# Kernel optimization log

Measured on AMD Instinct MI355X. Metric: run time of the kernel, lower is better.

The kernel has to match this reference:

```python
import jax, jax.numpy as jnp
import numpy as np

B, C, H, W = 16, 128, 64, 64
LN_EPS = 1e-5


def _gru_dir(x, w_ih, w_hh, b_ih, b_hh, reverse):
    # x: [N, T, C]; PyTorch GRU cell math:
    # r = sig(Wir x + bir + Whr h + bhr); z = sig(Wiz x + biz + Whz h + bhz)
    xp = jnp.einsum('ntc,gc->ntg', x, w_ih) + b_ih  # [N,T,3C] precomputed input gates
    xs = jnp.swapaxes(xp, 0, 1)  # [T,N,3C]
    h0 = jnp.zeros((x.shape[0], w_hh.shape[1]), x.dtype)

    def step(h, xt):
        g = h @ w_hh.T + b_hh
        xr, xz, xn = jnp.split(xt, 3, axis=-1)
        hr, hz, hn = jnp.split(g, 3, axis=-1)
        r = jax.nn.sigmoid(xr + hr)
        z = jax.nn.sigmoid(xz + hz)
        n = jnp.tanh(xn + r * hn)
        h2 = (1.0 - z) * n + z * h
        return h2, h2

    _, ys = jax.lax.scan(step, h0, xs, reverse=reverse)
    return jnp.swapaxes(ys, 0, 1)  # [N,T,C]


def _gru_bidir(x, wih_f, whh_f, bih_f, bhh_f, wih_b, whh_b, bib_b, bhh_b):
    of = _gru_dir(x, wih_f, whh_f, bih_f, bhh_f, False)
    ob = _gru_dir(x, wih_b, whh_b, bib_b, bhh_b, True)
    return jnp.concatenate([of, ob], axis=-1)  # [N,T,2C]


def _forward(x, ln_g, ln_b,
             h_wih_f, h_whh_f, h_bih_f, h_bhh_f,
             h_wih_b, h_whh_b, h_bih_b, h_bhh_b,
             w_wih_f, w_whh_f, w_bih_f, w_bhh_f,
             w_wih_b, w_whh_b, w_bih_b, w_bhh_b,
             proj_w, proj_b):
    Bn, Cc, Hh, Ww = x.shape
    x_flat = x.reshape(Bn, Cc, Hh * Ww).transpose(0, 2, 1)  # b (h w) c
    mu = x_flat.mean(-1, keepdims=True)
    var = ((x_flat - mu) ** 2).mean(-1, keepdims=True)
    xn = (x_flat - mu) * jax.lax.rsqrt(var + LN_EPS) * ln_g + ln_b
    x4 = xn.reshape(Bn, Hh, Ww, Cc)
    # horizontal scan: rows as batch, sequence along W
    x_h = x4.reshape(Bn * Hh, Ww, Cc)
    out_h = _gru_bidir(x_h, h_wih_f, h_whh_f, h_bih_f, h_bhh_f,
                       h_wih_b, h_whh_b, h_bih_b, h_bhh_b)
    out_h = out_h.reshape(Bn, Hh * Ww, 2 * Cc)
    # vertical scan: cols as batch, sequence along H
    x_v = x4.transpose(0, 2, 1, 3).reshape(Bn * Ww, Hh, Cc)
    out_v = _gru_bidir(x_v, w_wih_f, w_whh_f, w_bih_f, w_bhh_f,
                       w_wih_b, w_whh_b, w_bih_b, w_bhh_b)
    out_v = out_v.reshape(Bn, Ww, Hh, 2 * Cc).transpose(0, 2, 1, 3).reshape(Bn, Hh * Ww, 2 * Cc)
    out = jnp.concatenate([out_h, out_v], axis=-1) @ proj_w.T + proj_b
    out = out + x_flat  # dropout in eval mode = identity
    return out.transpose(0, 2, 1).reshape(Bn, Cc, Hh, Ww)


def setup_inputs():
    key = jax.random.key(0)
    key, kx = jax.random.split(key)
    d = {
        'x': jax.random.normal(kx, (B, C, H, W), jnp.float32),
        'ln_g': jnp.ones((C,), jnp.float32),
        'ln_b': jnp.zeros((C,), jnp.float32),
    }
    bound = 1.0 / np.sqrt(C)  # torch GRU init: U(-1/sqrt(hidden), 1/sqrt(hidden))
    shapes = {'wih': (3 * C, C), 'whh': (3 * C, C), 'bih': (3 * C,), 'bhh': (3 * C,)}
    for pre in ('h', 'w'):
        for dr in ('f', 'b'):
            for p, sh in shapes.items():
                key, k1 = jax.random.split(key)
                d[f'{pre}_{p}_{dr}'] = jax.random.uniform(k1, sh, jnp.float32, -bound, bound)
    bp = 1.0 / np.sqrt(4 * C)
    key, k1, k2 = jax.random.split(key, 3)
    d['proj_w'] = jax.random.uniform(k1, (C, 4 * C), jnp.float32, -bp, bp)
    d['proj_b'] = jax.random.uniform(k2, (C,), jnp.float32, -bp, bp)
    return d


def reference(x, ln_g, ln_b,
              h_wih_f, h_whh_f, h_bih_f, h_bhh_f,
              h_wih_b, h_whh_b, h_bih_b, h_bhh_b,
              w_wih_f, w_whh_f, w_bih_f, w_bhh_f,
              w_wih_b, w_whh_b, w_bih_b, w_bhh_b,
              proj_w, proj_b):
    return _forward(x, ln_g, ln_b,
                    h_wih_f, h_whh_f, h_bih_f, h_bhh_f,
                    h_wih_b, h_whh_b, h_bih_b, h_bhh_b,
                    w_wih_f, w_whh_f, w_bih_f, w_bhh_f,
                    w_wih_b, w_whh_b, w_bih_b, w_bhh_b,
                    proj_w, proj_b)
```

## Files before the change

kernel.cpp:

```cpp
#include <hip/hip_runtime.h>

typedef short bf16x8 __attribute__((ext_vector_type(8)));
typedef float f32x4 __attribute__((ext_vector_type(4)));

static __device__ __forceinline__ unsigned short f2bf(float f) {
  unsigned u = __builtin_bit_cast(unsigned, f);
  u += 0x7FFFu + ((u >> 16) & 1u);
  return (unsigned short)(u >> 16);
}

static __device__ __forceinline__ bf16x8 pack8s(const float* p, float s) {
  float4 a = *(const float4*)p;
  float4 b = *(const float4*)(p + 4);
  bf16x8 r;
  r[0] = (short)f2bf(a.x * s); r[1] = (short)f2bf(a.y * s);
  r[2] = (short)f2bf(a.z * s); r[3] = (short)f2bf(a.w * s);
  r[4] = (short)f2bf(b.x * s); r[5] = (short)f2bf(b.y * s);
  r[6] = (short)f2bf(b.z * s); r[7] = (short)f2bf(b.w * s);
  return r;
}

#define NLOG2E -1.442695040888963f
#define N2LOG2E -2.885390081777927f

__global__ __launch_bounds__(512) void pwprep_kernel(
    const float* __restrict__ pw, unsigned short* __restrict__ pwb) {
  const int i = blockIdx.x * 512 + threadIdx.x;
  pwb[i] = f2bf(pw[i]);
}

__global__ __launch_bounds__(512, 2) void ln_kernel(
    const float* __restrict__ x, const float* __restrict__ lg,
    const float* __restrict__ lb, unsigned short* __restrict__ xn) {
  __shared__ __align__(16) unsigned char slds[35840];
  float* mu_s = (float*)(slds + 34816);
  float* rs_s = (float*)(slds + 35328);
  const int tid = threadIdx.x;
  const int bid = blockIdx.x;
  const int b = bid >> 5;
  const int hw0 = (bid & 31) << 7;
  const int q = tid >> 5, slot = tid & 31;
  const int lane = tid & 63, wv = tid >> 6;

  const float* xbase = x + ((size_t)b * 128) * 4096 + hw0 + (slot << 2);
  float4 xv[8];
#pragma unroll
  for (int p = 0; p < 8; ++p)
    xv[p] = *(const float4*)(xbase + (size_t)(q * 8 + p) * 4096);

  float s1[4] = {0.f, 0.f, 0.f, 0.f}, s2[4] = {0.f, 0.f, 0.f, 0.f};
#pragma unroll
  for (int p = 0; p < 8; ++p) {
    s1[0] += xv[p].x; s2[0] = fmaf(xv[p].x, xv[p].x, s2[0]);
    s1[1] += xv[p].y; s2[1] = fmaf(xv[p].y, xv[p].y, s2[1]);
    s1[2] += xv[p].z; s2[2] = fmaf(xv[p].z, xv[p].z, s2[2]);
    s1[3] += xv[p].w; s2[3] = fmaf(xv[p].w, xv[p].w, s2[3]);
  }
#pragma unroll
  for (int j = 0; j < 4; ++j) {
    s1[j] += __shfl_xor(s1[j], 32);
    s2[j] += __shfl_xor(s2[j], 32);
  }
  if (lane < 32) {
    float* psp = (float*)(slds + (wv * 32 + slot) * 36);
#pragma unroll
    for (int j = 0; j < 4; ++j) { psp[j] = s1[j]; psp[4 + j] = s2[j]; }
  }
  __syncthreads();
  if (tid < 128) {
    const int sl2 = tid >> 2, j2 = tid & 3;
    float a1 = 0.f, a2 = 0.f;
#pragma unroll
    for (int w = 0; w < 8; ++w) {
      const float* psp = (const float*)(slds + (w * 32 + sl2) * 36);
      a1 += psp[j2]; a2 += psp[4 + j2];
    }
    const float mu = a1 * 0.0078125f;
    const float var = a2 * 0.0078125f - mu * mu;
    mu_s[tid] = mu;
    rs_s[tid] = rsqrtf(var + 1e-5f);
  }
  __syncthreads();

  float lgv[8], lbv[8];
#pragma unroll
  for (int p = 0; p < 8; ++p) { lgv[p] = lg[q * 8 + p]; lbv[p] = lb[q * 8 + p]; }
#pragma unroll
  for (int j = 0; j < 4; ++j) {
    const int pos = (slot << 2) + j;
    const float mu = mu_s[pos], rs = rs_s[pos];
    float y[8];
#pragma unroll
    for (int p = 0; p < 8; ++p) {
      const float xvj = j == 0 ? xv[p].x : j == 1 ? xv[p].y : j == 2 ? xv[p].z : xv[p].w;
      y[p] = (xvj - mu) * rs * lgv[p] + lbv[p];
    }
    unsigned h0, h1, h2, h3;
    asm("v_cvt_pk_bf16_f32 %0, %1, %2" : "=v"(h0) : "v"(y[0]), "v"(y[1]));
    asm("v_cvt_pk_bf16_f32 %0, %1, %2" : "=v"(h1) : "v"(y[2]), "v"(y[3]));
    asm("v_cvt_pk_bf16_f32 %0, %1, %2" : "=v"(h2) : "v"(y[4]), "v"(y[5]));
    asm("v_cvt_pk_bf16_f32 %0, %1, %2" : "=v"(h3) : "v"(y[6]), "v"(y[7]));
    uint4 v; v.x = h0; v.y = h1; v.z = h2; v.w = h3;
    *(uint4*)(slds + pos * 272 + (q << 4)) = v;
  }
  __syncthreads();
#pragma unroll
  for (int it = 0; it < 4; ++it) {
    const int idx = (it << 9) + tid;
    const int row = idx >> 4, g = idx & 15;
    uint4 v = *(const uint4*)(slds + row * 272 + (g << 4));
    *(uint4*)((unsigned char*)xn + ((size_t)(b * 4096 + hw0 + row)) * 256 + (g << 4)) = v;
  }
}

__global__ __launch_bounds__(512, 2) void scan_kernel(
    const unsigned short* __restrict__ xn, unsigned short* __restrict__ cat,
    const float* __restrict__ wih0, const float* __restrict__ whh0,
    const float* __restrict__ bih0, const float* __restrict__ bhh0,
    const float* __restrict__ wih1, const float* __restrict__ whh1,
    const float* __restrict__ bih1, const float* __restrict__ bhh1,
    const float* __restrict__ wih2, const float* __restrict__ whh2,
    const float* __restrict__ bih2, const float* __restrict__ bhh2,
    const float* __restrict__ wih3, const float* __restrict__ whh3,
    const float* __restrict__ bih3, const float* __restrict__ bhh3) {
  __shared__ __align__(16) unsigned char lds[16384];
  const int tid = threadIdx.x;
  const int bid = blockIdx.x;
  const int dir = bid >> 6;
  const int grp = bid & 63;
  const int fwd = !(dir & 1);
  const int vert = dir >> 1;
  const int b = grp >> 2;
  const int r0 = (grp & 3) << 4;
  const int wv = tid >> 6;
  const int lane = tid & 63;
  const int l15 = lane & 15;
  const int l4 = lane >> 4;

  const float* wih = dir == 0 ? wih0 : dir == 1 ? wih1 : dir == 2 ? wih2 : wih3;
  const float* whh = dir == 0 ? whh0 : dir == 1 ? whh1 : dir == 2 ? whh2 : whh3;
  const float* bih = dir == 0 ? bih0 : dir == 1 ? bih1 : dir == 2 ? bih2 : bih3;
  const float* bhh = dir == 0 ? bhh0 : dir == 1 ? bhh1 : dir == 2 ? bhh2 : bhh3;

  const int ca = (wv << 4) + l15;
  bf16x8 wf[3][2][4];
#pragma unroll
  for (int g = 0; g < 3; ++g) {
    const float sc = g == 2 ? N2LOG2E : NLOG2E;
#pragma unroll
    for (int s = 0; s < 2; ++s) {
      const float* Wp = s ? whh : wih;
#pragma unroll
      for (int kc = 0; kc < 4; ++kc)
        wf[g][s][kc] = pack8s(Wp + (size_t)((g << 7) + ca) * 128 + (kc << 5) + (l4 << 3), sc);
    }
  }
  const int cb = (wv << 4) + (l4 << 2);
  f32x4 br4, bz4, bnx4, bnh4;
  {
    float4 a = *(const float4*)(bih + cb), b2 = *(const float4*)(bhh + cb);
    br4[0] = (a.x + b2.x) * NLOG2E; br4[1] = (a.y + b2.y) * NLOG2E;
    br4[2] = (a.z + b2.z) * NLOG2E; br4[3] = (a.w + b2.w) * NLOG2E;
    a = *(const float4*)(bih + 128 + cb); b2 = *(const float4*)(bhh + 128 + cb);
    bz4[0] = (a.x + b2.x) * NLOG2E; bz4[1] = (a.y + b2.y) * NLOG2E;
    bz4[2] = (a.z + b2.z) * NLOG2E; bz4[3] = (a.w + b2.w) * NLOG2E;
    a = *(const float4*)(bih + 256 + cb);
    bnx4[0] = a.x * N2LOG2E; bnx4[1] = a.y * N2LOG2E;
    bnx4[2] = a.z * N2LOG2E; bnx4[3] = a.w * N2LOG2E;
    b2 = *(const float4*)(bhh + 256 + cb);
    bnh4[0] = b2.x * N2LOG2E; bnh4[1] = b2.y * N2LOG2E;
    bnh4[2] = b2.z * N2LOG2E; bnh4[3] = b2.w * N2LOG2E;
  }

  const int ss = tid >> 4, ck = tid & 15;
  const unsigned char* xsp =
      (const unsigned char*)xn +
      (vert ? ((size_t)b << 20) + (size_t)(r0 + ss) * 256 + (ck << 4)
            : ((size_t)(b * 64 + r0 + ss) << 14) + (ck << 4));
  const int xstep = vert ? 16384 : 256;
  const int sdst = (ss * 256 + (ck << 4)) ^ ((ss & 15) << 4);

  const int seq = r0 + l15;
  const int cstep = vert ? 65536 : 1024;
  unsigned char* catp =
      (unsigned char*)cat +
      ((size_t)b * 4096 + (size_t)(vert ? seq : seq * 64)) * 1024 + dir * 256 + (cb << 1) +
      (size_t)(fwd ? 0 : 63) * cstep;
  const int cdelta = fwd ? cstep : -cstep;

  *(unsigned long long*)(lds + 8192 + tid * 8) = 0ull;
  f32x4 hst = {0.f, 0.f, 0.f, 0.f};

  uint4 sX, sY;
  f32x4 grA, gzA, gnxA, grB, gzB, gnxB;
  {
    const unsigned char* xlq =
        (const unsigned char*)xn +
        (vert ? ((size_t)b << 20) + (size_t)(fwd ? 0 : 63) * 16384 + (size_t)seq * 256
              : ((size_t)(b * 64 + seq) << 14) + (size_t)(fwd ? 0 : 63) * 256) +
        (l4 << 4);
    bf16x8 x0[4];
#pragma unroll
    for (int kc = 0; kc < 4; ++kc) x0[kc] = *(const bf16x8*)(xlq + (kc << 6));
    uint4 s1v;
    if (tid < 256) {
      s1v = *(const uint4*)(xsp + (fwd ? 1 : 62) * xstep);
      sX = *(const uint4*)(xsp + (fwd ? 2 : 61) * xstep);
    }
    grA = br4; gzA = bz4; gnxA = bnx4;
#pragma unroll
    for (int kc = 0; kc < 4; ++kc) {
      grA = __builtin_amdgcn_mfma_f32_16x16x32_bf16(wf[0][0][kc], x0[kc], grA, 0, 0, 0);
      gzA = __builtin_amdgcn_mfma_f32_16x16x32_bf16(wf[1][0][kc], x0[kc], gzA, 0, 0, 0);
      gnxA = __builtin_amdgcn_mfma_f32_16x16x32_bf16(wf[2][0][kc], x0[kc], gnxA, 0, 0, 0);
    }
    if (tid < 256) *(uint4*)(lds + 4096 + sdst) = s1v;
  }
  __syncthreads();

#define STEP(TT, HCUR, HNXT, XRD, XWR, XW, XL, GRC, GZC, GNXC, GRN, GZN, GNXN)  \
  {                                                                             \
    bf16x8 ha[4], xa[4];                                                        \
    _Pragma("unroll")                                                           \
    for (int kc = 0; kc < 4; ++kc) {                                            \
      const int base = (l15 * 256 + (kc << 6) + (l4 << 4)) ^ (l15 << 4);        \
      ha[kc] = *(const bf16x8*)(lds + (HCUR) + base);                           \
      xa[kc] = *(const bf16x8*)(lds + (XRD) + base);                            \
    }                                                                           \
    if (tid < 256) {                                                            \
      *(uint4*)(lds + (XWR) + sdst) = XW;                                       \
      const int tl = (TT) + 3 > 63 ? 63 : (TT) + 3;                             \
      XL = *(const uint4*)(xsp + (fwd ? tl : 63 - tl) * xstep);                 \
    }                                                                           \
    f32x4 rh = {0.f, 0.f, 0.f, 0.f}, zh = {0.f, 0.f, 0.f, 0.f}, nh = bnh4;     \
    _Pragma("unroll")                                                           \
    for (int kc = 0; kc < 4; ++kc) {                                            \
      rh = __builtin_amdgcn_mfma_f32_16x16x32_bf16(wf[0][1][kc], ha[kc], rh, 0, 0, 0); \
      zh = __builtin_amdgcn_mfma_f32_16x16x32_bf16(wf[1][1][kc], ha[kc], zh, 0, 0, 0); \
      nh = __builtin_amdgcn_mfma_f32_16x16x32_bf16(wf[2][1][kc], ha[kc], nh, 0, 0, 0); \
    }                                                                           \
    GRN = br4; GZN = bz4; GNXN = bnx4;                                          \
    _Pragma("unroll")                                                           \
    for (int kc = 0; kc < 4; ++kc) {                                            \
      GRN = __builtin_amdgcn_mfma_f32_16x16x32_bf16(wf[0][0][kc], xa[kc], GRN, 0, 0, 0); \
      GZN = __builtin_amdgcn_mfma_f32_16x16x32_bf16(wf[1][0][kc], xa[kc], GZN, 0, 0, 0); \
      GNXN = __builtin_amdgcn_mfma_f32_16x16x32_bf16(wf[2][0][kc], xa[kc], GNXN, 0, 0, 0); \
    }                                                                           \
    f32x4 hnew;                                                                 \
    _Pragma("unroll")                                                           \
    for (int r = 0; r < 4; ++r) {                                               \
      const float er = __builtin_amdgcn_exp2f(GRC[r] + rh[r]);                  \
      const float rr = __builtin_amdgcn_rcpf(1.f + er);                         \
      const float ez = __builtin_amdgcn_exp2f(GZC[r] + zh[r]);                  \
      const float zz = __builtin_amdgcn_rcpf(1.f + ez);                         \
      const float pre = GNXC[r] + rr * nh[r];                                   \
      const float e2 = __builtin_amdgcn_exp2f(pre);                             \
      const float nn = fmaf(2.f, __builtin_amdgcn_rcpf(1.f + e2), -1.f);        \
      hnew[r] = nn + zz * (hst[r] - nn);                                        \
    }                                                                           \
    hst = hnew;                                                                 \
    unsigned hp0, hp1;                                                          \
    asm("v_cvt_pk_bf16_f32 %0, %1, %2" : "=v"(hp0) : "v"(hnew[0]), "v"(hnew[1])); \
    asm("v_cvt_pk_bf16_f32 %0, %1, %2" : "=v"(hp1) : "v"(hnew[2]), "v"(hnew[3])); \
    {                                                                           \
      unsigned long long hp = (unsigned long long)hp0 | ((unsigned long long)hp1 << 32); \
      *(unsigned long long*)(lds + (HNXT) + ((l15 * 256 + (cb << 1)) ^ (l15 << 4))) = hp; \
    }                                                                           \
    {                                                                           \
      uint2 v; v.x = hp0; v.y = hp1;                                            \
      *(uint2*)catp = v;                                                        \
      catp += cdelta;                                                           \
    }                                                                           \
    asm volatile("s_waitcnt lgkmcnt(0)" ::: "memory");                          \
    __builtin_amdgcn_s_barrier();                                               \
    asm volatile("" ::: "memory");                                              \
  }

  for (int tt2 = 0; tt2 < 64; tt2 += 2) {
    STEP(tt2, 8192, 12288, 4096, 0, sX, sY, grA, gzA, gnxA, grB, gzB, gnxB);
    STEP(tt2 + 1, 12288, 8192, 0, 4096, sY, sX, grB, gzB, gnxB, grA, gzA, gnxA);
  }
#undef STEP
}

__global__ __launch_bounds__(512, 4) void proj_kernel(
    const unsigned short* __restrict__ cat, const unsigned short* __restrict__ pwb,
    const float* __restrict__ pb, const float* __restrict__ x,
    float* __restrict__ out) {
  __shared__ __align__(16) unsigned char lds[33280];
  const int tid = threadIdx.x;
  const int bid = blockIdx.x;
  const int row0 = bid << 6;
  const int b = row0 >> 12;
  const int hw0 = row0 & 4095;
  const int wv = tid >> 6, lane = tid & 63, l15 = lane & 15, l4 = lane >> 4;

  const int cc = (wv << 4) + l15;
  bf16x8 wfr[16];
#pragma unroll
  for (int kc = 0; kc < 16; ++kc)
    wfr[kc] = *(const bf16x8*)(pwb + (size_t)cc * 512 + (kc << 5) + (l4 << 3));
  const float pbv = pb[cc];

  f32x4 acc[4];
#pragma unroll
  for (int mt = 0; mt < 4; ++mt) acc[mt] = {pbv, pbv, pbv, pbv};

#pragma unroll
  for (int s = 0; s < 2; ++s) {
#pragma unroll
    for (int it = 0; it < 4; ++it) {
      const int item = tid + (it << 9);
      const int rr = item >> 6, ckk = item & 63;
      uint4 v = *(const uint4*)((const unsigned char*)cat +
                                ((size_t)(row0 + (s << 5) + rr)) * 1024 + ckk * 16);
      *(uint4*)(lds + rr * 1024 + ((ckk ^ (rr & 7)) << 4)) = v;
    }
    __syncthreads();
#pragma unroll
    for (int mh = 0; mh < 2; ++mh) {
      const int mt = (s << 1) + mh;
      const int rl = (mh << 4) + l15;
#pragma unroll
      for (int kc = 0; kc < 16; ++kc) {
        bf16x8 af =
            *(const bf16x8*)(lds + rl * 1024 + ((((kc << 2) + l4) ^ (rl & 7)) << 4));
        acc[mt] = __builtin_amdgcn_mfma_f32_16x16x32_bf16(af, wfr[kc], acc[mt], 0, 0, 0);
      }
    }
    __syncthreads();
  }

#pragma unroll
  for (int mt = 0; mt < 4; ++mt)
#pragma unroll
    for (int j = 0; j < 4; ++j)
      *(float*)(lds + cc * 260 + (((mt << 4) + (l4 << 2) + j) << 2)) = acc[mt][j];
  __syncthreads();
#pragma unroll
  for (int it = 0; it < 16; ++it) {
    const int c = (wv << 4) + it;
    const float v = *(const float*)(lds + c * 260 + (lane << 2));
    const size_t off = (size_t)(b * 128 + c) * 4096 + hw0 + lane;
    out[off] = v + x[off];
  }
}

extern "C" void kernel_launch(void* const* d_in, const int* in_sizes, int n_in,
                              void* d_out, int out_size, void* d_ws, size_t ws_size,
                              hipStream_t stream) {
  const float* x = (const float*)d_in[0];
  const float* lg = (const float*)d_in[1];
  const float* lb = (const float*)d_in[2];
  unsigned short* xn = (unsigned short*)d_ws;
  unsigned short* cat =
      (unsigned short*)((unsigned char*)d_ws + 16777216);
  unsigned short* pwb =
      (unsigned short*)((unsigned char*)d_ws + 16777216 + 67108864);

  pwprep_kernel<<<128, 512, 0, stream>>>((const float*)d_in[19], pwb);
  ln_kernel<<<512, 512, 0, stream>>>(x, lg, lb, xn);
  scan_kernel<<<256, 512, 0, stream>>>(
      xn, cat,
      (const float*)d_in[3], (const float*)d_in[4], (const float*)d_in[5], (const float*)d_in[6],
      (const float*)d_in[7], (const float*)d_in[8], (const float*)d_in[9], (const float*)d_in[10],
      (const float*)d_in[11], (const float*)d_in[12], (const float*)d_in[13], (const float*)d_in[14],
      (const float*)d_in[15], (const float*)d_in[16], (const float*)d_in[17], (const float*)d_in[18]);
  proj_kernel<<<1024, 512, 0, stream>>>(cat, pwb, (const float*)d_in[20], x,
                                        (float*)d_out);
}
```

Before: 118.8 us.

## Halve scan block to 4 waves, each computing two 16-channel tiles

The GRU scan kernel now launches 256 threads per block instead of 512, and each wave handles 32 hidden channels (two MFMA tiles) instead of 16. Weight fragments, biases, hidden state and gate accumulators are duplicated per wave, and all threads now take part in staging the next x slice. The aim is to cut the per-step barrier cost, since fewer waves synchronise on each of the 64 serial steps, and to give each wave more independent MFMAs to interleave. In exchange, register pressure roughly doubles (launch bounds now 256,1), and there are half as many waves per CU to hide latency.

Result: slower. 126.8 us (+6.8%).

```diff
diff --git a/kernel.cpp b/kernel.cpp
--- a/kernel.cpp
+++ b/kernel.cpp
@@ -113,7 +113,7 @@
   }
 }
 
-__global__ __launch_bounds__(512, 2) void scan_kernel(
+__global__ __launch_bounds__(256, 1) void scan_kernel(
     const unsigned short* __restrict__ xn, unsigned short* __restrict__ cat,
     const float* __restrict__ wih0, const float* __restrict__ whh0,
     const float* __restrict__ bih0, const float* __restrict__ bhh0,
@@ -142,8 +142,8 @@
   const float* bih = dir == 0 ? bih0 : dir == 1 ? bih1 : dir == 2 ? bih2 : bih3;
   const float* bhh = dir == 0 ? bhh0 : dir == 1 ? bhh1 : dir == 2 ? bhh2 : bhh3;
 
-  const int ca = (wv << 4) + l15;
-  bf16x8 wf[3][2][4];
+  const int caA = (wv << 5) + l15;
+  bf16x8 wfA[3][2][4], wfB[3][2][4];
 #pragma unroll
   for (int g = 0; g < 3; ++g) {
     const float sc = g == 2 ? N2LOG2E : NLOG2E;
@@ -151,25 +151,40 @@
     for (int s = 0; s < 2; ++s) {
       const float* Wp = s ? whh : wih;
 #pragma unroll
-      for (int kc = 0; kc < 4; ++kc)
-        wf[g][s][kc] = pack8s(Wp + (size_t)((g << 7) + ca) * 128 + (kc << 5) + (l4 << 3), sc);
-    }
-  }
-  const int cb = (wv << 4) + (l4 << 2);
-  f32x4 br4, bz4, bnx4, bnh4;
+      for (int kc = 0; kc < 4; ++kc) {
+        wfA[g][s][kc] = pack8s(Wp + (size_t)((g << 7) + caA) * 128 + (kc << 5) + (l4 << 3), sc);
+        wfB[g][s][kc] = pack8s(Wp + (size_t)((g << 7) + caA + 16) * 128 + (kc << 5) + (l4 << 3), sc);
+      }
+    }
+  }
+  const int cbA = (wv << 5) + (l4 << 2);
+  const int cbB = cbA + 16;
+  f32x4 brA, bzA, bnxA, bnhA, brB, bzB, bnxB, bnhB;
   {
-    float4 a = *(const float4*)(bih + cb), b2 = *(const float4*)(bhh + cb);
-    br4[0] = (a.x + b2.x) * NLOG2E; br4[1] = (a.y + b2.y) * NLOG2E;
-    br4[2] = (a.z + b2.z) * NLOG2E; br4[3] = (a.w + b2.w) * NLOG2E;
-    a = *(const float4*)(bih + 128 + cb); b2 = *(const float4*)(bhh + 128 + cb);
-    bz4[0] = (a.x + b2.x) * NLOG2E; bz4[1] = (a.y + b2.y) * NLOG2E;
-    bz4[2] = (a.z + b2.z) * NLOG2E; bz4[3] = (a.w + b2.w) * NLOG2E;
-    a = *(const float4*)(bih + 256 + cb);
-    bnx4[0] = a.x * N2LOG2E; bnx4[1] = a.y * N2LOG2E;
-    bnx4[2] = a.z * N2LOG2E; bnx4[3] = a.w * N2LOG2E;
-    b2 = *(const float4*)(bhh + 256 + cb);
-    bnh4[0] = b2.x * N2LOG2E; bnh4[1] = b2.y * N2LOG2E;
-    bnh4[2] = b2.z * N2LOG2E; bnh4[3] = b2.w * N2LOG2E;
+    float4 a = *(const float4*)(bih + cbA), c = *(const float4*)(bhh + cbA);
+    brA[0] = (a.x + c.x) * NLOG2E; brA[1] = (a.y + c.y) * NLOG2E;
+    brA[2] = (a.z + c.z) * NLOG2E; brA[3] = (a.w + c.w) * NLOG2E;
+    a = *(const float4*)(bih + cbB); c = *(const float4*)(bhh + cbB);
+    brB[0] = (a.x + c.x) * NLOG2E; brB[1] = (a.y + c.y) * NLOG2E;
+    brB[2] = (a.z + c.z) * NLOG2E; brB[3] = (a.w + c.w) * NLOG2E;
+    a = *(const float4*)(bih + 128 + cbA); c = *(const float4*)(bhh + 128 + cbA);
+    bzA[0] = (a.x + c.x) * NLOG2E; bzA[1] = (a.y + c.y) * NLOG2E;
+    bzA[2] = (a.z + c.z) * NLOG2E; bzA[3] = (a.w + c.w) * NLOG2E;
+    a = *(const float4*)(bih + 128 + cbB); c = *(const float4*)(bhh + 128 + cbB);
+    bzB[0] = (a.x + c.x) * NLOG2E; bzB[1] = (a.y + c.y) * NLOG2E;
+    bzB[2] = (a.z + c.z) * NLOG2E; bzB[3] = (a.w + c.w) * NLOG2E;
+    a = *(const float4*)(bih + 256 + cbA);
+    bnxA[0] = a.x * N2LOG2E; bnxA[1] = a.y * N2LOG2E;
+    bnxA[2] = a.z * N2LOG2E; bnxA[3] = a.w * N2LOG2E;
+    a = *(const float4*)(bih + 256 + cbB);
+    bnxB[0] = a.x * N2LOG2E; bnxB[1] = a.y * N2LOG2E;
+    bnxB[2] = a.z * N2LOG2E; bnxB[3] = a.w * N2LOG2E;
+    c = *(const float4*)(bhh + 256 + cbA);
+    bnhA[0] = c.x * N2LOG2E; bnhA[1] = c.y * N2LOG2E;
+    bnhA[2] = c.z * N2LOG2E; bnhA[3] = c.w * N2LOG2E;
+    c = *(const float4*)(bhh + 256 + cbB);
+    bnhB[0] = c.x * N2LOG2E; bnhB[1] = c.y * N2LOG2E;
+    bnhB[2] = c.z * N2LOG2E; bnhB[3] = c.w * N2LOG2E;
   }
 
   const int ss = tid >> 4, ck = tid & 15;
@@ -184,15 +199,19 @@
   const int cstep = vert ? 65536 : 1024;
   unsigned char* catp =
       (unsigned char*)cat +
-      ((size_t)b * 4096 + (size_t)(vert ? seq : seq * 64)) * 1024 + dir * 256 + (cb << 1) +
+      ((size_t)b * 4096 + (size_t)(vert ? seq : seq * 64)) * 1024 + dir * 256 + (cbA << 1) +
       (size_t)(fwd ? 0 : 63) * cstep;
   const int cdelta = fwd ? cstep : -cstep;
 
-  *(unsigned long long*)(lds + 8192 + tid * 8) = 0ull;
-  f32x4 hst = {0.f, 0.f, 0.f, 0.f};
+  {
+    uint4 z; z.x = 0; z.y = 0; z.z = 0; z.w = 0;
+    *(uint4*)(lds + 8192 + tid * 16) = z;
+  }
+  f32x4 hsA = {0.f, 0.f, 0.f, 0.f}, hsB = {0.f, 0.f, 0.f, 0.f};
 
   uint4 sX, sY;
-  f32x4 grA, gzA, gnxA, grB, gzB, gnxB;
+  f32x4 grPa, gzPa, gnxPa, grPb, gzPb, gnxPb;
+  f32x4 grQa, gzQa, gnxQa, grQb, gzQb, gnxQb;
   {
     const unsigned char* xlq =
         (const unsigned char*)xn +
@@ -203,22 +222,43 @@
 #pragma unroll
     for (int kc = 0; kc < 4; ++kc) x0[kc] = *(const bf16x8*)(xlq + (kc << 6));
     uint4 s1v;
-    if (tid < 256) {
-      s1v = *(const uint4*)(xsp + (fwd ? 1 : 62) * xstep);
-      sX = *(const uint4*)(xsp + (fwd ? 2 : 61) * xstep);
-    }
-    grA = br4; gzA = bz4; gnxA = bnx4;
+    s1v = *(const uint4*)(xsp + (fwd ? 1 : 62) * xstep);
+    sX = *(const uint4*)(xsp + (fwd ? 2 : 61) * xstep);
+    grPa = brA; gzPa = bzA; gnxPa = bnxA;
+    grPb = brB; gzPb = bzB; gnxPb = bnxB;
 #pragma unroll
     for (int kc = 0; kc < 4; ++kc) {
-      grA = __builtin_amdgcn_mfma_f32_16x16x32_bf16(wf[0][0][kc], x0[kc], grA, 0, 0, 0);
-      gzA = __builtin_amdgcn_mfma_f32_16x16x32_bf16(wf[1][0][kc], x0[kc], gzA, 0, 0, 0);
-      gnxA = __builtin_amdgcn_mfma_f32_16x16x32_bf16(wf[2][0][kc], x0[kc], gnxA, 0, 0, 0);
-    }
-    if (tid < 256) *(uint4*)(lds + 4096 + sdst) = s1v;
+      grPa = __builtin_amdgcn_mfma_f32_16x16x32_bf16(wfA[0][0][kc], x0[kc], grPa, 0, 0, 0);
+      grPb = __builtin_amdgcn_mfma_f32_16x16x32_bf16(wfB[0][0][kc], x0[kc], grPb, 0, 0, 0);
+      gzPa = __builtin_amdgcn_mfma_f32_16x16x32_bf16(wfA[1][0][kc], x0[kc], gzPa, 0, 0, 0);
+      gzPb = __builtin_amdgcn_mfma_f32_16x16x32_bf16(wfB[1][0][kc], x0[kc], gzPb, 0, 0, 0);
+      gnxPa = __builtin_amdgcn_mfma_f32_16x16x32_bf16(wfA[2][0][kc], x0[kc], gnxPa, 0, 0, 0);
+      gnxPb = __builtin_amdgcn_mfma_f32_16x16x32_bf16(wfB[2][0][kc], x0[kc], gnxPb, 0, 0, 0);
+    }
+    *(uint4*)(lds + 4096 + sdst) = s1v;
   }
   __syncthreads();
 
-#define STEP(TT, HCUR, HNXT, XRD, XWR, XW, XL, GRC, GZC, GNXC, GRN, GZN, GNXN)  \
+#define GATEBLK(GRC, GZC, GNXC, RH, ZH, NH, HS, HP0, HP1)                       \
+    f32x4 hnew_;                                                                \
+    _Pragma("unroll")                                                           \
+    for (int r = 0; r < 4; ++r) {                                               \
+      const float er = __builtin_amdgcn_exp2f(GRC[r] + RH[r]);                  \
+      const float rr = __builtin_amdgcn_rcpf(1.f + er);                         \
+      const float ez = __builtin_amdgcn_exp2f(GZC[r] + ZH[r]);                  \
+      const float zz = __builtin_amdgcn_rcpf(1.f + ez);                         \
+      const float pre = GNXC[r] + rr * NH[r];                                   \
+      const float e2 = __builtin_amdgcn_exp2f(pre);                             \
+      const float nn = fmaf(2.f, __builtin_amdgcn_rcpf(1.f + e2), -1.f);        \
+      hnew_[r] = nn + zz * (HS[r] - nn);                                        \
+    }                                                                           \
+    HS = hnew_;                                                                 \
+    asm("v_cvt_pk_bf16_f32 %0, %1, %2" : "=v"(HP0) : "v"(hnew_[0]), "v"(hnew_[1])); \
+    asm("v_cvt_pk_bf16_f32 %0, %1, %2" : "=v"(HP1) : "v"(hnew_[2]), "v"(hnew_[3]));
+
+#define STEP(TT, HCUR, HNXT, XRD, XWR, XW, XL,                                  \
+             GRCa, GZCa, GNXCa, GRCb, GZCb, GNXCb,                              \
+             GRNa, GZNa, GNXNa, GRNb, GZNb, GNXNb)                              \
   {                                                                             \
     bf16x8 ha[4], xa[4];                                                        \
     _Pragma("unroll")                                                           \
@@ -227,48 +267,49 @@
       ha[kc] = *(const bf16x8*)(lds + (HCUR) + base);                           \
       xa[kc] = *(const bf16x8*)(lds + (XRD) + base);                            \
     }                                                                           \
-    if (tid < 256) {                                                            \
-      *(uint4*)(lds + (XWR) + sdst) = XW;                                       \
+    *(uint4*)(lds + (XWR) + sdst) = XW;                                         \
+    {                                                                           \
       const int tl = (TT) + 3 > 63 ? 63 : (TT) + 3;                             \
       XL = *(const uint4*)(xsp + (fwd ? tl : 63 - tl) * xstep);                 \
     }                                                                           \
-    f32x4 rh = {0.f, 0.f, 0.f, 0.f}, zh = {0.f, 0.f, 0.f, 0.f}, nh = bnh4;     \
+                              \
+    f32x4 rha = {0.f, 0.f, 0.f, 0.f}, zha = {0.f, 0.f, 0.f, 0.f}, nha = bnhA;   \
+    f32x4 rhb = {0.f, 0.f, 0.f, 0.f}, zhb = {0.f, 0.f, 0.f, 0.f}, nhb = bnhB;   \
     _Pragma("unroll")                                                           \
     for (int kc = 0; kc < 4; ++kc) {                                            \
-      rh = __builtin_amdgcn_mfma_f32_16x16x32_bf16(wf[0][1][kc], ha[kc], rh, 0, 0, 0); \
-      zh = __builtin_amdgcn_mfma_f32_16x16x32_bf16(wf[1][1][kc], ha[kc], zh, 0, 0, 0); \
-      nh = __builtin_amdgcn_mfma_f32_16x16x32_bf16(wf[2][1][kc], ha[kc], nh, 0, 0, 0); \
-    }                                                                           \
-    GRN = br4; GZN = bz4; GNXN = bnx4;                                          \
+      rha = __builtin_amdgcn_mfma_f32_16x16x32_bf16(wfA[0][1][kc], ha[kc], rha, 0, 0, 0); \
+      rhb = __builtin_amdgcn_mfma_f32_16x16x32_bf16(wfB[0][1][kc], ha[kc], rhb, 0, 0, 0); \
+      zha = __builtin_amdgcn_mfma_f32_16x16x32_bf16(wfA[1][1][kc], ha[kc], zha, 0, 0, 0); \
+      zhb = __builtin_amdgcn_mfma_f32_16x16x32_bf16(wfB[1][1][kc], ha[kc], zhb, 0, 0, 0); \
+      nha = __builtin_amdgcn_mfma_f32_16x16x32_bf16(wfA[2][1][kc], ha[kc], nha, 0, 0, 0); \
+      nhb = __builtin_amdgcn_mfma_f32_16x16x32_bf16(wfB[2][1][kc], ha[kc], nhb, 0, 0, 0); \
+    }                                                                           \
+                                           \
+    GRNa = brA; GZNa = bzA; GNXNa = bnxA;                                       \
+    GRNb = brB; GZNb = bzB; GNXNb = bnxB;                                       \
     _Pragma("unroll")                                                           \
     for (int kc = 0; kc < 4; ++kc) {                                            \
-      GRN = __builtin_amdgcn_mfma_f32_16x16x32_bf16(wf[0][0][kc], xa[kc], GRN, 0, 0, 0); \
-      GZN = __builtin_amdgcn_mfma_f32_16x16x32_bf16(wf[1][0][kc], xa[kc], GZN, 0, 0, 0); \
-      GNXN = __builtin_amdgcn_mfma_f32_16x16x32_bf16(wf[2][0][kc], xa[kc], GNXN, 0, 0, 0); \
-    }                                                                           \
-    f32x4 hnew;                                                                 \
-    _Pragma("unroll")                                                           \
-    for (int r = 0; r < 4; ++r) {                                               \
-      const float er = __builtin_amdgcn_exp2f(GRC[r] + rh[r]);                  \
-      const float rr = __builtin_amdgcn_rcpf(1.f + er);                         \
-      const float ez = __builtin_amdgcn_exp2f(GZC[r] + zh[r]);                  \
-      const float zz = __builtin_amdgcn_rcpf(1.f + ez);                         \
-      const float pre = GNXC[r] + rr * nh[r];                                   \
-      const float e2 = __builtin_amdgcn_exp2f(pre);                             \
-      const float nn = fmaf(2.f, __builtin_amdgcn_rcpf(1.f + e2), -1.f);        \
-      hnew[r] = nn + zz * (hst[r] - nn);                                        \
-    }                                                                           \
-    hst = hnew;                                                                 \
-    unsigned hp0, hp1;                                                          \
-    asm("v_cvt_pk_bf16_f32 %0, %1, %2" : "=v"(hp0) : "v"(hnew[0]), "v"(hnew[1])); \
-    asm("v_cvt_pk_bf16_f32 %0, %1, %2" : "=v"(hp1) : "v"(hnew[2]), "v"(hnew[3])); \
+      GRNa = __builtin_amdgcn_mfma_f32_16x16x32_bf16(wfA[0][0][kc], xa[kc], GRNa, 0, 0, 0); \
+      GRNb = __builtin_amdgcn_mfma_f32_16x16x32_bf16(wfB[0][0][kc], xa[kc], GRNb, 0, 0, 0); \
+      GZNa = __builtin_amdgcn_mfma_f32_16x16x32_bf16(wfA[1][0][kc], xa[kc], GZNa, 0, 0, 0); \
+      GZNb = __builtin_amdgcn_mfma_f32_16x16x32_bf16(wfB[1][0][kc], xa[kc], GZNb, 0, 0, 0); \
+      GNXNa = __builtin_amdgcn_mfma_f32_16x16x32_bf16(wfA[2][0][kc], xa[kc], GNXNa, 0, 0, 0); \
+      GNXNb = __builtin_amdgcn_mfma_f32_16x16x32_bf16(wfB[2][0][kc], xa[kc], GNXNb, 0, 0, 0); \
+    }                                                                           \
+    unsigned hpa0, hpa1, hpb0, hpb1;                                            \
+    { GATEBLK(GRCa, GZCa, GNXCa, rha, zha, nha, hsA, hpa0, hpa1) }              \
+    { GATEBLK(GRCb, GZCb, GNXCb, rhb, zhb, nhb, hsB, hpb0, hpb1) }              \
     {                                                                           \
-      unsigned long long hp = (unsigned long long)hp0 | ((unsigned long long)hp1 << 32); \
-      *(unsigned long long*)(lds + (HNXT) + ((l15 * 256 + (cb << 1)) ^ (l15 << 4))) = hp; \
+      unsigned long long hpA = (unsigned long long)hpa0 | ((unsigned long long)hpa1 << 32); \
+      unsigned long long hpB = (unsigned long long)hpb0 | ((unsigned long long)hpb1 << 32); \
+      *(unsigned long long*)(lds + (HNXT) + ((l15 * 256 + (cbA << 1)) ^ (l15 << 4))) = hpA; \
+      *(unsigned long long*)(lds + (HNXT) + ((l15 * 256 + (cbB << 1)) ^ (l15 << 4))) = hpB; \
     }                                                                           \
     {                                                                           \
-      uint2 v; v.x = hp0; v.y = hp1;                                            \
-      *(uint2*)catp = v;                                                        \
+      uint2 va; va.x = hpa0; va.y = hpa1;                                       \
+      uint2 vb; vb.x = hpb0; vb.y = hpb1;                                       \
+      *(uint2*)catp = va;                                                       \
+      *(uint2*)(catp + 32) = vb;                                                \
       catp += cdelta;                                                           \
     }                                                                           \
     asm volatile("s_waitcnt lgkmcnt(0)" ::: "memory");                          \
@@ -277,10 +318,15 @@
   }
 
   for (int tt2 = 0; tt2 < 64; tt2 += 2) {
-    STEP(tt2, 8192, 12288, 4096, 0, sX, sY, grA, gzA, gnxA, grB, gzB, gnxB);
-    STEP(tt2 + 1, 12288, 8192, 0, 4096, sY, sX, grB, gzB, gnxB, grA, gzA, gnxA);
+    STEP(tt2, 8192, 12288, 4096, 0, sX, sY,
+         grPa, gzPa, gnxPa, grPb, gzPb, gnxPb,
+         grQa, gzQa, gnxQa, grQb, gzQb, gnxQb);
+    STEP(tt2 + 1, 12288, 8192, 0, 4096, sY, sX,
+         grQa, gzQa, gnxQa, grQb, gzQb, gnxQb,
+         grPa, gzPa, gnxPa, grPb, gzPb, gnxPb);
   }
 #undef STEP
+#undef GATEBLK
 }
 
 __global__ __launch_bounds__(512, 4) void proj_kernel(
@@ -360,7 +406,7 @@
 
   pwprep_kernel<<<128, 512, 0, stream>>>((const float*)d_in[19], pwb);
   ln_kernel<<<512, 512, 0, stream>>>(x, lg, lb, xn);
-  scan_kernel<<<256, 512, 0, stream>>>(
+  scan_kernel<<<256, 256, 0, stream>>>(
       xn, cat,
       (const float*)d_in[3], (const float*)d_in[4], (const float*)d_in[5], (const float*)d_in[6],
       (const float*)d_in[7], (const float*)d_in[8], (const float*)d_in[9], (const float*)d_in[10],
```
